# Performance work log

Hardware: AMD Instinct MI355X
Metric: run time of the kernel (lower is better)

Reference implementation:

```python
import jax, jax.numpy as jnp
import numpy as np

IN_CH = 64
OUT_CH = 32
SCALE = 2
BLOCK = SCALE ** 3  # 8
N = 400000   # input sparse voxels (lines in pair_fwd)
M = 200000   # output sparse voxels


def setup_inputs() -> dict:
    key = jax.random.key(0)
    k1, k2, k3 = jax.random.split(key, 3)
    x_features = jax.random.normal(k1, (N, IN_CH), dtype=jnp.float32)
    # flat ParameterList: weights[i*BLOCK + j] is the (in_channels,) weight for
    # output channel i, kernel position j
    weights = jax.random.normal(k2, (BLOCK * OUT_CH, IN_CH), dtype=jnp.float32)
    # spconv pair_fwd: [kernel_volume, num_lines], -1 marks invalid mapping
    pair_fwd = jax.random.randint(k3, (BLOCK, N), -1, M)
    return {"x_features": x_features, "weights": weights,
            "pair_fwd": pair_fwd, "num_out": M}


def reference(x_features, weights, pair_fwd, num_out):
    block, n = pair_fwd.shape
    out_ch = weights.shape[0] // block
    # W[o, j, c] == weights_list[o*block + j]
    W = weights.reshape(out_ch, block, -1)
    # sequential VoxelShuffle then .view(-1) per block is identity on each
    # voxel's in_channels feature vector, so:
    # vals[j, n, o] = dot(W[o, j, :], x_features[n, :])
    vals = jnp.einsum('nc,ojc->jno', x_features, W)  # [block, N, out_ch]
    idx = pair_fwd.reshape(-1)                       # [block*N]
    # route invalid (-1) entries to a dummy trailing row
    safe = jnp.where(idx >= 0, idx, num_out)
    buf = jnp.zeros((num_out + 1, out_ch), dtype=vals.dtype)
    # original uses assignment (set) semantics into out_features
    buf = buf.at[safe].set(vals.reshape(block * n, out_ch))
    return buf[:num_out]
```

## Files before the change

### kernel.cpp

```cpp
#include <hip/hip_runtime.h>

#define IN_CH  64
#define OUT_CH 32
#define BLOCK  8
#define ROWS   8


__device__ __forceinline__ float bflo(unsigned u) { return __uint_as_float(u << 16); }
__device__ __forceinline__ float bfhi(unsigned u) { return __uint_as_float(u & 0xffff0000u); }

__global__ void k_prep(const float* __restrict__ w, unsigned* __restrict__ wt,
                       int4* __restrict__ argmax4, int n4) {
    int i = blockIdx.x * 256 + threadIdx.x;
    if (i < n4) argmax4[i] = make_int4(-1, -1, -1, -1);
    if (i < BLOCK * OUT_CH * IN_CH / 2) {
        int q  = i & 3;
        int o  = (i >> 2) & 31;
        int j  = (i >> 7) & 7;
        int c8 = i >> 10;
        int c  = c8 * 8 + q * 2;
        float f0 = w[(o * BLOCK + j) * IN_CH + c];
        float f1 = w[(o * BLOCK + j) * IN_CH + c + 1];
        auto cvt = [](float f) -> unsigned {
            unsigned u = __float_as_uint(f);
            return (u + 0x7fffu + ((u >> 16) & 1u)) >> 16;
        };
        wt[i] = cvt(f0) | (cvt(f1) << 16);
    }
}

__global__ void k_scatter_range(const int* __restrict__ pair, int* __restrict__ argmax,
                                int N, int jhi, int jlo, int flip) {
    int n = blockIdx.x * 256 + threadIdx.x;
    if (n >= N) return;
    if (flip) n = N - 1 - n;
    for (int j = jhi; j >= jlo; --j) {
        int t = j * N + n;
        int m = pair[t];
        if (m >= 0 && argmax[m] < t)
            atomicMax(&argmax[m], t);
    }
}

__device__ __forceinline__ float row_dot(const float* __restrict__ buf, int r, int jcv,
                                         const uint4* __restrict__ Wl, int o, int h) {
    const float4* xp = (const float4*)(buf + r * 64) + h * 8;
    const uint4*  wp = Wl + h * 1024 + (jcv & 7) * 32 + o;
    float ax = 0.f, ay = 0.f, az = 0.f, aw = 0.f;
#pragma unroll
    for (int k = 0; k < 4; ++k) {
        uint4  wq  = wp[k * 256];
        float4 xv0 = xp[k * 2];
        float4 xv1 = xp[k * 2 + 1];
        ax = fmaf(bflo(wq.x), xv0.x, ax);
        ay = fmaf(bfhi(wq.x), xv0.y, ay);
        az = fmaf(bflo(wq.y), xv0.z, az);
        aw = fmaf(bfhi(wq.y), xv0.w, aw);
        ax = fmaf(bflo(wq.z), xv1.x, ax);
        ay = fmaf(bfhi(wq.z), xv1.y, ay);
        az = fmaf(bflo(wq.w), xv1.z, az);
        aw = fmaf(bfhi(wq.w), xv1.w, aw);
    }
    float s = (ax + ay) + (az + aw);
    s += __shfl_xor(s, 32);
    return (jcv == 8) ? 0.f : s;
}

__global__ __launch_bounds__(512, 4) void k_compute(
        const float* __restrict__ x, const uint4* __restrict__ wt,
        const int* __restrict__ argmax, float* __restrict__ out, int M, int N) {
    __shared__ uint4 Wl[2048];
    __shared__ __align__(16) float Xl[8][2][ROWS * 64];
    for (int i = threadIdx.x; i < 2048; i += 512) Wl[i] = wt[i];
    __syncthreads();

    const int lane = threadIdx.x & 63;
    const int o    = lane & 31;
    const int h    = lane >> 5;
    const int wv   = threadIdx.x >> 6;
    const unsigned uN = (unsigned)N;

    int gw   = blockIdx.x * 8 + wv;
    int base = gw * 64;
    if (base >= M) return;
    int nrows = min(64, M - base);

    int t0 = ((base + lane) < M) ? argmax[base + lane] : -1;
    int jn = 8, nn = 0;
    if (t0 >= 0) {
        unsigned j = (unsigned)t0 / uN;
        nn = t0 - (int)(j * uN);
        jn = (int)j;
    }

    int ntiles = (nrows + ROWS - 1) / ROWS;
    float ld[ROWS];

#pragma unroll
    for (int r = 0; r < ROWS; ++r) {
        int n = __builtin_amdgcn_readlane(nn, r);
        ld[r] = x[(size_t)n * IN_CH + lane];
    }

    for (int tile = 0; tile < ntiles; ++tile) {
        float* buf = &Xl[wv][tile & 1][0];

        int jc[ROWS];
#pragma unroll
        for (int r = 0; r < ROWS; ++r)
            jc[r] = __builtin_amdgcn_readlane(jn, tile * ROWS + r);

#pragma unroll
        for (int r = 0; r < ROWS; ++r)
            buf[r * 64 + lane] = ld[r];

        if (tile + 1 < ntiles) {
            int nb = (tile + 1) * ROWS;
#pragma unroll
            for (int r = 0; r < ROWS; ++r) {
                int n = __builtin_amdgcn_readlane(nn, nb + r);
                ld[r] = x[(size_t)n * IN_CH + lane];
            }
        }

        asm volatile("s_waitcnt lgkmcnt(0)" ::: "memory");

#pragma unroll
        for (int r = 0; r < ROWS; r += 2) {
            int grow = tile * ROWS + r;
            float s0 = row_dot(buf, r,     jc[r],     Wl, o, h);
            float s1 = row_dot(buf, r + 1, jc[r + 1], Wl, o, h);
            float sv   = h ? s1 : s0;
            int   orow = grow + h;
            if (orow < nrows)
                out[(size_t)(base + orow) * OUT_CH + o] = sv;
        }
    }
}

extern "C" void kernel_launch(void* const* d_in, const int* in_sizes, int n_in,
                              void* d_out, int out_size, void* d_ws, size_t ws_size,
                              hipStream_t stream) {
    const float* x    = (const float*)d_in[0];
    const float* w    = (const float*)d_in[1];
    const int*   pair = (const int*)d_in[2];
    int N = in_sizes[0] / IN_CH;
    int M = out_size / OUT_CH;

    char*     ws     = (char*)d_ws;
    int*      argmax = (int*)ws;
    unsigned* wt     = (unsigned*)(ws + (size_t)M * 4);

    int n4 = M / 4;
    k_prep<<<(n4 + 255) / 256, 256, 0, stream>>>(w, wt, (int4*)argmax, n4);

    int gN = (N + 255) / 256;
    k_scatter_range<<<gN, 256, 0, stream>>>(pair, argmax, N, 7, 7, 1);
    k_scatter_range<<<gN, 256, 0, stream>>>(pair, argmax, N, 6, 0, 0);

    int waves  = (M + 63) / 64;
    int blocks = (waves + 7) / 8;
    k_compute<<<blocks, 512, 0, stream>>>(x, (const uint4*)wt, argmax,
                                          (float*)d_out, M, N);
}
```

Measured before the change: 96.34 us.

## Bucket output rows by kernel position and keep fp32 weights in registers

Adds a k_fill pass that groups output rows into per-kernel-position buckets using a block-local histogram and global atomic cursors. The compute kernel then gives each wave 64 rows sharing one kernel position, so that position's fp32 weight slice can sit in registers. This drops the bf16 weight staging in shared memory and the per-row weight gather. It costs an extra kernel launch, extra index arrays and atomics, and scattered output writes where contiguous stores were before.

Result: slower. 99.79 us (+3.6%).

```diff
diff --git a/kernel.cpp b/kernel.cpp
--- a/kernel.cpp
+++ b/kernel.cpp
@@ -6,27 +6,10 @@
 #define ROWS   8
 
 
-__device__ __forceinline__ float bflo(unsigned u) { return __uint_as_float(u << 16); }
-__device__ __forceinline__ float bfhi(unsigned u) { return __uint_as_float(u & 0xffff0000u); }
-
-__global__ void k_prep(const float* __restrict__ w, unsigned* __restrict__ wt,
-                       int4* __restrict__ argmax4, int n4) {
+__global__ void k_prep(int4* __restrict__ argmax4, int n4, int* __restrict__ cur) {
     int i = blockIdx.x * 256 + threadIdx.x;
+    if (i < 16) cur[i] = 0;
     if (i < n4) argmax4[i] = make_int4(-1, -1, -1, -1);
-    if (i < BLOCK * OUT_CH * IN_CH / 2) {
-        int q  = i & 3;
-        int o  = (i >> 2) & 31;
-        int j  = (i >> 7) & 7;
-        int c8 = i >> 10;
-        int c  = c8 * 8 + q * 2;
-        float f0 = w[(o * BLOCK + j) * IN_CH + c];
-        float f1 = w[(o * BLOCK + j) * IN_CH + c + 1];
-        auto cvt = [](float f) -> unsigned {
-            unsigned u = __float_as_uint(f);
-            return (u + 0x7fffu + ((u >> 16) & 1u)) >> 16;
-        };
-        wt[i] = cvt(f0) | (cvt(f1) << 16);
-    }
 }
 
 __global__ void k_scatter_range(const int* __restrict__ pair, int* __restrict__ argmax,
@@ -42,56 +25,61 @@
     }
 }
 
-__device__ __forceinline__ float row_dot(const float* __restrict__ buf, int r, int jcv,
-                                         const uint4* __restrict__ Wl, int o, int h) {
-    const float4* xp = (const float4*)(buf + r * 64) + h * 8;
-    const uint4*  wp = Wl + h * 1024 + (jcv & 7) * 32 + o;
-    float ax = 0.f, ay = 0.f, az = 0.f, aw = 0.f;
-#pragma unroll
-    for (int k = 0; k < 4; ++k) {
-        uint4  wq  = wp[k * 256];
-        float4 xv0 = xp[k * 2];
-        float4 xv1 = xp[k * 2 + 1];
-        ax = fmaf(bflo(wq.x), xv0.x, ax);
-        ay = fmaf(bfhi(wq.x), xv0.y, ay);
-        az = fmaf(bflo(wq.y), xv0.z, az);
-        aw = fmaf(bfhi(wq.y), xv0.w, aw);
-        ax = fmaf(bflo(wq.z), xv1.x, ax);
-        ay = fmaf(bfhi(wq.z), xv1.y, ay);
-        az = fmaf(bflo(wq.w), xv1.z, az);
-        aw = fmaf(bfhi(wq.w), xv1.w, aw);
+__global__ void k_fill(const int* __restrict__ argmax, int* __restrict__ cur,
+                       int* __restrict__ bm, int* __restrict__ bn, int M, int N) {
+    __shared__ int h9[9];
+    __shared__ int b9[9];
+    if (threadIdx.x < 9) h9[threadIdx.x] = 0;
+    __syncthreads();
+    int m = blockIdx.x * 256 + threadIdx.x;
+    int j = 9, n = 0, lo = 0;
+    if (m < M) {
+        int t = argmax[m];
+        if (t >= 0) { j = (int)((unsigned)t / (unsigned)N); n = t - j * N; }
+        else j = 8;
+        lo = atomicAdd(&h9[j], 1);
     }
-    float s = (ax + ay) + (az + aw);
-    s += __shfl_xor(s, 32);
-    return (jcv == 8) ? 0.f : s;
+    __syncthreads();
+    if (threadIdx.x < 9 && h9[threadIdx.x] > 0)
+        b9[threadIdx.x] = atomicAdd(&cur[threadIdx.x], h9[threadIdx.x]);
+    __syncthreads();
+    if (m < M) {
+        int pos = j * M + b9[j] + lo;
+        bm[pos] = m;
+        bn[pos] = n;
+    }
 }
 
 __global__ __launch_bounds__(512, 4) void k_compute(
-        const float* __restrict__ x, const uint4* __restrict__ wt,
-        const int* __restrict__ argmax, float* __restrict__ out, int M, int N) {
-    __shared__ uint4 Wl[2048];
+        const float* __restrict__ x, const float* __restrict__ w,
+        const int* __restrict__ cnt, const int* __restrict__ bm,
+        const int* __restrict__ bn, float* __restrict__ out, int M, int N) {
     __shared__ __align__(16) float Xl[8][2][ROWS * 64];
-    for (int i = threadIdx.x; i < 2048; i += 512) Wl[i] = wt[i];
-    __syncthreads();
 
     const int lane = threadIdx.x & 63;
     const int o    = lane & 31;
-    const int h    = lane >> 5;
+    const int hh   = lane >> 5;
     const int wv   = threadIdx.x >> 6;
-    const unsigned uN = (unsigned)N;
 
-    int gw   = blockIdx.x * 8 + wv;
-    int base = gw * 64;
-    if (base >= M) return;
-    int nrows = min(64, M - base);
+    int T = blockIdx.x * 8 + wv;
+    int j = 0, nrows = 0;
+    for (; j < 9; ++j) {
+        int c  = cnt[j];
+        int nt = (c + 63) >> 6;
+        if (T < nt) { nrows = min(64, c - T * 64); break; }
+        T -= nt;
+    }
+    if (j >= 9) return;
+    int base = j * M + T * 64;
 
-    int t0 = ((base + lane) < M) ? argmax[base + lane] : -1;
-    int jn = 8, nn = 0;
-    if (t0 >= 0) {
-        unsigned j = (unsigned)t0 / uN;
-        nn = t0 - (int)(j * uN);
-        jn = (int)j;
-    }
+    int jw = (j < 8) ? j : 0;
+    float4 wreg[8];
+#pragma unroll
+    for (int k = 0; k < 8; ++k)
+        wreg[k] = *(const float4*)&w[(o * BLOCK + jw) * IN_CH + hh * 32 + k * 4];
+
+    int mm = 0, nn = 0;
+    if (lane < nrows) { mm = bm[base + lane]; nn = bn[base + lane]; }
 
     int ntiles = (nrows + ROWS - 1) / ROWS;
     float ld[ROWS];
@@ -104,12 +92,6 @@
 
     for (int tile = 0; tile < ntiles; ++tile) {
         float* buf = &Xl[wv][tile & 1][0];
-
-        int jc[ROWS];
-#pragma unroll
-        for (int r = 0; r < ROWS; ++r)
-            jc[r] = __builtin_amdgcn_readlane(jn, tile * ROWS + r);
-
 #pragma unroll
         for (int r = 0; r < ROWS; ++r)
             buf[r * 64 + lane] = ld[r];
@@ -128,12 +110,31 @@
 #pragma unroll
         for (int r = 0; r < ROWS; r += 2) {
             int grow = tile * ROWS + r;
-            float s0 = row_dot(buf, r,     jc[r],     Wl, o, h);
-            float s1 = row_dot(buf, r + 1, jc[r + 1], Wl, o, h);
-            float sv   = h ? s1 : s0;
-            int   orow = grow + h;
+            float s01[2];
+#pragma unroll
+            for (int p = 0; p < 2; ++p) {
+                const float4* xp = (const float4*)(buf + (r + p) * 64) + hh * 8;
+                float ax = 0.f, ay = 0.f, az = 0.f, aw = 0.f;
+#pragma unroll
+                for (int k = 0; k < 8; ++k) {
+                    float4 xv = xp[k];
+                    ax = fmaf(wreg[k].x, xv.x, ax);
+                    ay = fmaf(wreg[k].y, xv.y, ay);
+                    az = fmaf(wreg[k].z, xv.z, az);
+                    aw = fmaf(wreg[k].w, xv.w, aw);
+                }
+                float s = (ax + ay) + (az + aw);
+                s += __shfl_xor(s, 32);
+                s01[p] = s;
+            }
+            float sv   = hh ? s01[1] : s01[0];
+            int   m0   = __builtin_amdgcn_readlane(mm, grow);
+            int   m1   = __builtin_amdgcn_readlane(mm, grow + 1);
+            int   mrow = hh ? m1 : m0;
+            if (j == 8) sv = 0.f;
+            int orow = grow + hh;
             if (orow < nrows)
-                out[(size_t)(base + orow) * OUT_CH + o] = sv;
+                out[(size_t)mrow * OUT_CH + o] = sv;
         }
     }
 }
@@ -147,19 +148,22 @@
     int N = in_sizes[0] / IN_CH;
     int M = out_size / OUT_CH;
 
-    char*     ws     = (char*)d_ws;
-    int*      argmax = (int*)ws;
-    unsigned* wt     = (unsigned*)(ws + (size_t)M * 4);
+    char* ws     = (char*)d_ws;
+    int*  cur    = (int*)ws;
+    int*  argmax = (int*)(ws + 256);
+    int*  bm     = (int*)(ws + 256 + (size_t)M * 4);
+    int*  bn     = (int*)(ws + 256 + (size_t)M * 4 + (size_t)9 * M * 4);
 
     int n4 = M / 4;
-    k_prep<<<(n4 + 255) / 256, 256, 0, stream>>>(w, wt, (int4*)argmax, n4);
+    k_prep<<<(n4 + 255) / 256, 256, 0, stream>>>((int4*)argmax, n4, cur);
 
     int gN = (N + 255) / 256;
     k_scatter_range<<<gN, 256, 0, stream>>>(pair, argmax, N, 7, 7, 1);
     k_scatter_range<<<gN, 256, 0, stream>>>(pair, argmax, N, 6, 0, 0);
 
-    int waves  = (M + 63) / 64;
-    int blocks = (waves + 7) / 8;
-    k_compute<<<blocks, 512, 0, stream>>>(x, (const uint4*)wt, argmax,
-                                          (float*)d_out, M, N);
+    k_fill<<<(M + 255) / 256, 256, 0, stream>>>(argmax, cur, bm, bn, M, N);
+
+    int maxtiles = (M + 63) / 64 + 8;
+    int blocks   = (maxtiles + 7) / 8;
+    k_compute<<<blocks, 512, 0, stream>>>(x, w, cur, bm, bn, (float*)d_out, M, N);
 }
```
